# Kernel tuning notes

Hardware: AMD Instinct MI355X
Metric: run time of the kernel (lower is better)

The kernel has to match this reference:

```python
import math
import jax, jax.numpy as jnp
import numpy as np

B, C, HI, WI = 64, 3, 224, 224
H, W, UR, UT = 32, 64, 10, 10
R_MIN, R_MAX = 0.01, 0.6


def setup_inputs() -> dict:
    key = jax.random.key(0)
    kx, kl = jax.random.split(key)
    # log-spaced radii and uniform angles -> polar sample grid [Hg, Wg, 2] (x, y)
    sample_r = np.exp(np.linspace(math.log(R_MIN), math.log(R_MAX), UR * H)).astype(np.float32)
    angles = (2.0 * np.pi * np.arange(W * UT) / (W * UT)).astype(np.float32)
    grid_2d = np.stack(
        [sample_r[:, None] * np.cos(angles)[None, :],
         sample_r[:, None] * np.sin(angles)[None, :]], axis=-1
    ).astype(np.float32)
    x = jax.random.normal(kx, (B, C, HI, WI), dtype=jnp.float32)
    l_t_prev = jax.random.uniform(kl, (B, 2), minval=-0.3, maxval=0.3, dtype=jnp.float32)
    return {"x": x, "l_t_prev": l_t_prev, "grid_2d": jnp.asarray(grid_2d)}


def _grid_sample_bilinear_zeros(x, grid):
    # x: [B,C,Hi,Wi]; grid: [B,Hg,Wg,2] normalized (x,y) in [-1,1]
    # matches torch.grid_sample(mode='bilinear', padding_mode='zeros', align_corners=False)
    _, _, Hi, Wi = x.shape
    gx, gy = grid[..., 0], grid[..., 1]
    ix = ((gx + 1.0) * Wi - 1.0) * 0.5
    iy = ((gy + 1.0) * Hi - 1.0) * 0.5
    x0 = jnp.floor(ix)
    y0 = jnp.floor(iy)
    fx = ix - x0
    fy = iy - y0
    x0i = x0.astype(jnp.int32)
    y0i = y0.astype(jnp.int32)

    def gather(img, yy, xx):  # img [C,Hi,Wi]; yy,xx [Hg,Wg]
        return img[:, yy, xx]  # [C,Hg,Wg]

    out = jnp.zeros((x.shape[0], x.shape[1]) + grid.shape[1:3], dtype=x.dtype)
    for dy in (0, 1):
        for dx in (0, 1):
            xi = x0i + dx
            yi = y0i + dy
            wgt = (fx if dx else (1.0 - fx)) * (fy if dy else (1.0 - fy))
            valid = (xi >= 0) & (xi < Wi) & (yi >= 0) & (yi < Hi)
            xc = jnp.clip(xi, 0, Wi - 1)
            yc = jnp.clip(yi, 0, Hi - 1)
            v = jax.vmap(gather)(x, yc, xc)  # [B,C,Hg,Wg]
            out = out + v * (wgt * valid.astype(x.dtype))[:, None, :, :]
    return out


def reference(x, l_t_prev, grid_2d):
    # shift polar grid by glimpse center
    grid = l_t_prev[:, None, None, :] + grid_2d[None]  # [B,Hg,Wg,2]
    sampled = _grid_sample_bilinear_zeros(x, grid)      # [B,C,Hg,Wg]
    b, c, hg, wg = sampled.shape
    # AvgPool2d with kernel [UR, UT], stride [UR, UT]
    pooled = sampled.reshape(b, c, hg // UR, UR, wg // UT, UT).mean(axis=(3, 5))
    return pooled  # [B,C,H,W]
```

## Files before the change

kernel.cpp:

```cpp
#include <hip/hip_runtime.h>

#define Bx 64
#define Cx 3
#define HIx 224
#define WIx 224
#define HWx (HIx*WIx)
#define Hx 32
#define Wx 64
#define SECT 16
#define LDS_PX 3584

__device__ __forceinline__ unsigned f2bf(float f) {
    unsigned u = __float_as_uint(f);
    return ((u + 0x7fffu + ((u >> 16) & 1u)) >> 16);
}
__device__ __forceinline__ float bf_lo(unsigned u) { return __uint_as_float(u << 16); }
__device__ __forceinline__ float bf_hi(unsigned u) { return __uint_as_float(u & 0xffff0000u); }

__global__ __launch_bounds__(256)
void sample_analytic(const float* __restrict__ xg,
                     const float* __restrict__ lt,
                     float* __restrict__ out) {
    __shared__ uint2 tile[LDS_PX];

    int bx = blockIdx.x;
    int b   = bx >> 4;
    int sec = bx & 15;

    float lx = lt[2 * b];
    float ly = lt[2 * b + 1];
    float cxc = fmaf(lx, 112.f, 111.5f);
    float cyc = fmaf(ly, 112.f, 111.5f);

    const float DTH = 0.00981747704f;
    float t0a = (float)(40 * sec)      * DTH;
    float t1a = (float)(40 * sec + 39) * DTH;
    float c0s = __cosf(t0a), s0s = __sinf(t0a);
    float c1s = __cosf(t1a), s1s = __sinf(t1a);
    const float rA = 1.12f, rB = 67.2f;
    float xa = rA * c0s, xb_ = rA * c1s, xc = rB * c0s, xd = rB * c1s;
    float ya = rA * s0s, yb_ = rA * s1s, yc = rB * s0s, yd = rB * s1s;
    float xmn = fminf(fminf(xa, xb_), fminf(xc, xd));
    float xmx = fmaxf(fmaxf(xa, xb_), fmaxf(xc, xd));
    float ymn = fminf(fminf(ya, yb_), fminf(yc, yd));
    float ymx = fmaxf(fmaxf(ya, yb_), fmaxf(yc, yd));
    int xlo = (int)floorf(cxc + xmn) - 1;
    int xhi = (int)floorf(cxc + xmx) + 2;
    int ylo = (int)floorf(cyc + ymn) - 1;
    int yhi = (int)floorf(cyc + ymx) + 2;
    int Wb = (xhi - xlo + 1) | 1;

    int wid  = threadIdx.x >> 6;
    int lane = threadIdx.x & 63;
    const float* xb0 = xg + (size_t)b * Cx * HWx;
    for (int y = ylo + wid; y <= yhi; y += 4) {
        const float* row = xb0 + y * WIx;
        int lbase = (y - ylo) * Wb - xlo;
        for (int x = xlo + lane; x <= xhi; x += 64) {
            float v0 = row[x];
            float v1 = row[x + HWx];
            float v2 = row[x + 2 * HWx];
            uint2 p;
            p.x = f2bf(v0) | (f2bf(v1) << 16);
            p.y = f2bf(v2);
            tile[lbase + x] = p;
        }
    }
    __syncthreads();

    int lane2 = threadIdx.x & 1;
    int pxi = threadIdx.x >> 1;
    int oh = pxi >> 2;
    int ow = sec * 4 + (pxi & 3);

    const float DL = 0.0128349359f;
    const float L0 = -4.60517019f;
    float R0p = 112.f * __expf(fmaf((float)(oh * 10), DL, L0));
    const float KG[10] = {1.f,          1.01291766f, 1.02600217f, 1.03925572f, 1.05268048f,
                          1.06627866f,  1.08005247f, 1.09400417f, 1.10813601f, 1.12245030f};
    float rr[10];
#pragma unroll
    for (int gi = 0; gi < 10; ++gi) rr[gi] = R0p * KG[gi];

    float th0 = (float)(ow * 10) * DTH;
    float cth = __cosf(th0), sth = __sinf(th0);
    const float C[10] = {1.f,         0.99995181f, 0.99980724f, 0.99956631f, 0.99922903f,
                         0.99879546f, 0.99826561f, 0.99763955f, 0.99691733f, 0.99609904f};
    const float S[10] = {0.f,         0.00981732f, 0.01963369f, 0.02944817f, 0.03925982f,
                         0.04906767f, 0.05887080f, 0.06866826f, 0.07845910f, 0.08824237f};
    float u[5], v[5];
#pragma unroll
    for (int jp = 0; jp < 5; ++jp) {
        int jj = 2 * jp + lane2;
        u[jp] = fmaf(cth, C[jj], -sth * S[jj]);
        v[jp] = fmaf(sth, C[jj],  cth * S[jj]);
    }

    float cxl = cxc - (float)xlo;
    float cyl = cyc - (float)ylo;

    float a0 = 0.f, a1 = 0.f, a2 = 0.f;
#pragma unroll
    for (int gi = 0; gi < 10; ++gi) {
        float rg = rr[gi];
#pragma unroll
        for (int jp = 0; jp < 5; ++jp) {
            float ix = fmaf(rg, u[jp], cxl);
            float iy = fmaf(rg, v[jp], cyl);
            int x0 = (int)ix, y0 = (int)iy;
            float fx = ix - (float)x0;
            float fy = iy - (float)y0;
            const uint2* p = &tile[y0 * Wb + x0];
            uint2 q00 = p[0], q01 = p[1];
            uint2 q10 = p[Wb], q11 = p[Wb + 1];
            float m00 = fmaf(fx, bf_lo(q01.x) - bf_lo(q00.x), bf_lo(q00.x));
            float m01 = fmaf(fx, bf_hi(q01.x) - bf_hi(q00.x), bf_hi(q00.x));
            float m02 = fmaf(fx, bf_lo(q01.y) - bf_lo(q00.y), bf_lo(q00.y));
            float m10 = fmaf(fx, bf_lo(q11.x) - bf_lo(q10.x), bf_lo(q10.x));
            float m11 = fmaf(fx, bf_hi(q11.x) - bf_hi(q10.x), bf_hi(q10.x));
            float m12 = fmaf(fx, bf_lo(q11.y) - bf_lo(q10.y), bf_lo(q10.y));
            a0 += fmaf(fy, m10 - m00, m00);
            a1 += fmaf(fy, m11 - m01, m01);
            a2 += fmaf(fy, m12 - m02, m02);
        }
    }

    a0 += __shfl_xor(a0, 1);
    a1 += __shfl_xor(a1, 1);
    a2 += __shfl_xor(a2, 1);

    if (lane2 == 0) {
        const float sc = 0.01f;
        int obase = b * (Cx * Hx * Wx) + oh * Wx + ow;
        out[obase]               = a0 * sc;
        out[obase + Hx * Wx]     = a1 * sc;
        out[obase + 2 * Hx * Wx] = a2 * sc;
    }
}

extern "C" void kernel_launch(void* const* d_in, const int* in_sizes, int n_in,
                              void* d_out, int out_size, void* d_ws, size_t ws_size,
                              hipStream_t stream) {
    const float* x  = (const float*)d_in[0];
    const float* lt = (const float*)d_in[1];
    float* out = (float*)d_out;
    (void)d_ws; (void)ws_size;

    sample_analytic<<<Bx * SECT, 256, 0, stream>>>(x, lt, out);
}
```

Measured before the change: 99.73 us.

## Split each sector block into inner/outer radial halves with XCD-aware batch mapping

Doubles the grid to 2048 blocks by splitting each angular sector into an inner and an outer radial half. Each half stages a smaller bounding-box tile, and four threads now share an output pixel (two along radius, two along angle), with a two-step shuffle reduction. Block indices are remapped so that the blocks for one batch image land on the same XCD, which should improve L2 reuse of that image's input. The intent is more parallelism and less per-thread serial work, paid for with some overlapping input loads across the two halves and an extra shuffle.

```diff
diff --git a/kernel.cpp b/kernel.cpp
--- a/kernel.cpp
+++ b/kernel.cpp
@@ -7,8 +7,7 @@
 #define HWx (HIx*WIx)
 #define Hx 32
 #define Wx 64
-#define SECT 16
-#define LDS_PX 3584
+#define LDS_PX 3456
 
 __device__ __forceinline__ unsigned f2bf(float f) {
     unsigned u = __float_as_uint(f);
@@ -24,8 +23,12 @@
     __shared__ uint2 tile[LDS_PX];
 
     int bx = blockIdx.x;
-    int b   = bx >> 4;
-    int sec = bx & 15;
+    int xcd  = bx & 7;
+    int sub8 = (bx >> 3) & 7;
+    int b    = xcd * 8 + sub8;
+    int rest = bx >> 6;
+    int sec  = rest >> 1;
+    int h    = rest & 1;
 
     float lx = lt[2 * b];
     float ly = lt[2 * b + 1];
@@ -37,7 +40,8 @@
     float t1a = (float)(40 * sec + 39) * DTH;
     float c0s = __cosf(t0a), s0s = __sinf(t0a);
     float c1s = __cosf(t1a), s1s = __sinf(t1a);
-    const float rA = 1.12f, rB = 67.2f;
+    float rA = h ? 8.70f  : 1.12f;
+    float rB = h ? 67.2f  : 8.66f;
     float xa = rA * c0s, xb_ = rA * c1s, xc = rB * c0s, xd = rB * c1s;
     float ya = rA * s0s, yb_ = rA * s1s, yc = rB * s0s, yd = rB * s1s;
     float xmn = fminf(fminf(xa, xb_), fminf(xc, xd));
@@ -68,9 +72,10 @@
     }
     __syncthreads();
 
-    int lane2 = threadIdx.x & 1;
-    int pxi = threadIdx.x >> 1;
-    int oh = pxi >> 2;
+    int ap = threadIdx.x & 1;
+    int rp = (threadIdx.x >> 1) & 1;
+    int pxi = threadIdx.x >> 2;
+    int oh = h * 16 + (pxi >> 2);
     int ow = sec * 4 + (pxi & 3);
 
     const float DL = 0.0128349359f;
@@ -78,9 +83,9 @@
     float R0p = 112.f * __expf(fmaf((float)(oh * 10), DL, L0));
     const float KG[10] = {1.f,          1.01291766f, 1.02600217f, 1.03925572f, 1.05268048f,
                           1.06627866f,  1.08005247f, 1.09400417f, 1.10813601f, 1.12245030f};
-    float rr[10];
+    float rr[5];
 #pragma unroll
-    for (int gi = 0; gi < 10; ++gi) rr[gi] = R0p * KG[gi];
+    for (int k = 0; k < 5; ++k) rr[k] = R0p * (rp ? KG[2 * k + 1] : KG[2 * k]);
 
     float th0 = (float)(ow * 10) * DTH;
     float cth = __cosf(th0), sth = __sinf(th0);
@@ -91,7 +96,7 @@
     float u[5], v[5];
 #pragma unroll
     for (int jp = 0; jp < 5; ++jp) {
-        int jj = 2 * jp + lane2;
+        int jj = 2 * jp + ap;
         u[jp] = fmaf(cth, C[jj], -sth * S[jj]);
         v[jp] = fmaf(sth, C[jj],  cth * S[jj]);
     }
@@ -101,8 +106,8 @@
 
     float a0 = 0.f, a1 = 0.f, a2 = 0.f;
 #pragma unroll
-    for (int gi = 0; gi < 10; ++gi) {
-        float rg = rr[gi];
+    for (int k = 0; k < 5; ++k) {
+        float rg = rr[k];
 #pragma unroll
         for (int jp = 0; jp < 5; ++jp) {
             float ix = fmaf(rg, u[jp], cxl);
@@ -125,11 +130,11 @@
         }
     }
 
-    a0 += __shfl_xor(a0, 1);
-    a1 += __shfl_xor(a1, 1);
-    a2 += __shfl_xor(a2, 1);
+    a0 += __shfl_xor(a0, 1); a0 += __shfl_xor(a0, 2);
+    a1 += __shfl_xor(a1, 1); a1 += __shfl_xor(a1, 2);
+    a2 += __shfl_xor(a2, 1); a2 += __shfl_xor(a2, 2);
 
-    if (lane2 == 0) {
+    if ((threadIdx.x & 3) == 0) {
         const float sc = 0.01f;
         int obase = b * (Cx * Hx * Wx) + oh * Wx + ow;
         out[obase]               = a0 * sc;
@@ -146,5 +151,5 @@
     float* out = (float*)d_out;
     (void)d_ws; (void)ws_size;
 
-    sample_analytic<<<Bx * SECT, 256, 0, stream>>>(x, lt, out);
+    sample_analytic<<<2048, 256, 0, stream>>>(x, lt, out);
 }
```

New measurement: 96.03 us. 3.7% less time.
